# Kernel tuning notes

Measured on AMD Instinct MI355X. Metric: run time of the kernel, lower is better.

Reference implementation:

```python
import jax, jax.numpy as jnp
import numpy as np

N, C, K = 16384, 128, 20
C2, C8 = C // 2, C // 8
EPS = 1e-5  # torch BatchNorm default eps


def _bn(x, g, b, m, v):
    # inference-mode batchnorm over last (channel) axis
    return (x - m) * jax.lax.rsqrt(v + EPS) * g + b


def setup_inputs() -> dict:
    key = jax.random.key(0)
    ks = jax.random.split(key, 24)
    r = lambda i, sh, s=0.05: jax.random.normal(ks[i], sh, dtype=jnp.float32) * s
    u = lambda i, sh: jax.random.uniform(ks[i], sh, dtype=jnp.float32)
    return {
        "xyz": jax.random.normal(ks[0], (1, 3, N), dtype=jnp.float32),
        "features": jax.random.normal(ks[1], (1, C, N), dtype=jnp.float32),
        "w_mlp1": r(2, (C2, 6), 0.3), "b_mlp1": r(3, (C2,)),
        "bn1_g": u(4, (C2,)) * 0.5 + 0.75, "bn1_b": r(5, (C2,)),
        "bn1_m": r(6, (C2,)), "bn1_v": u(7, (C2,)) * 0.5 + 0.5,
        "w_mlp2": r(8, (C2, 2 * C), 0.06), "b_mlp2": r(9, (C2,)),
        "bn2_g": u(10, (C2,)) * 0.5 + 0.75, "bn2_b": r(11, (C2,)),
        "bn2_m": r(12, (C2,)), "bn2_v": u(13, (C2,)) * 0.5 + 0.5,
        "w_d1": r(14, (C8, C), 0.09), "w_d2": r(15, (C8, C), 0.09),
        "w_up": r(16, (C, C8), 0.25), "b_up": r(17, (C,)),
        "bnu_g": u(18, (C,)) * 0.5 + 0.75, "bnu_b": r(19, (C,)),
        "bnu_m": r(20, (C,)), "bnu_v": u(21, (C,)) * 0.5 + 0.5,
        "k": K,
    }


def reference(xyz, features, w_mlp1, b_mlp1, bn1_g, bn1_b, bn1_m, bn1_v,
              w_mlp2, b_mlp2, bn2_g, bn2_b, bn2_m, bn2_v,
              w_d1, w_d2, w_up, b_up, bnu_g, bnu_b, bnu_m, bnu_v, k):
    B = xyz.shape[0]
    xt = jnp.transpose(xyz, (0, 2, 1))        # [B,N,3]
    ft = jnp.transpose(features, (0, 2, 1))   # [B,N,C]
    # knn: pairwise_distance = -||xi||^2 + 2 xi.xj - ||xj||^2, topk = k nearest
    xx = jnp.sum(xyz * xyz, axis=1)           # [B,N]
    pd = 2.0 * jnp.einsum('bci,bcj->bij', xyz, xyz) - xx[:, :, None] - xx[:, None, :]
    _, idx = jax.lax.top_k(pd, k)             # [B,N,k]
    bidx = jnp.arange(B)[:, None, None]
    nbr_x = xt[bidx, idx]                     # [B,N,k,3]
    nbr_f = ft[bidx, idx]                     # [B,N,k,C]
    cx = xt[:, :, None, :]
    cf = ft[:, :, None, :]
    nx = jnp.concatenate([nbr_x - cx, jnp.broadcast_to(cx, nbr_x.shape)], axis=-1)  # [B,N,k,6]
    nf = jnp.concatenate([nbr_f - cf, jnp.broadcast_to(cf, nbr_f.shape)], axis=-1)  # [B,N,k,2C]
    hx = jax.nn.relu(_bn(jnp.einsum('bnkc,oc->bnko', nx, w_mlp1) + b_mlp1,
                         bn1_g, bn1_b, bn1_m, bn1_v))
    hf = jax.nn.relu(_bn(jnp.einsum('bnkc,oc->bnko', nf, w_mlp2) + b_mlp2,
                         bn2_g, bn2_b, bn2_m, bn2_v))
    f = jnp.max(jnp.concatenate([hx, hf], axis=-1), axis=2)   # [B,N,C]
    f1 = jax.nn.relu(jnp.einsum('bnc,oc->bno', f, w_d1))      # [B,N,C/8]
    f2 = jax.nn.relu(jnp.einsum('bnc,oc->bno', f, w_d2))      # [B,N,C/8]
    # faithful to original: .mean(...)[0] indexes batch 0 (valid since B==1)
    ch = jnp.mean(f1, axis=1)[0][:, None]     # [C/8,1]
    sp = jnp.mean(f2, axis=2)[0][None, :]     # [1,N]
    fe = jnp.sqrt(ch @ sp + 1e-12).T          # [N,C/8]
    fin = fe[None] + f1 + f2                  # [B,N,C/8]
    up = jax.nn.relu(_bn(jnp.einsum('bnc,oc->bno', fin, w_up) + b_up,
                         bnu_g, bnu_b, bnu_m, bnu_v))         # [B,N,C]
    fl = f - up
    fl = fl * jnp.tanh(jax.nn.softplus(fl))   # Mish
    return jnp.transpose(fl, (0, 2, 1))       # [B,C,N]
```

## Files before the change

### kernel.cpp

```cpp
#include <hip/hip_runtime.h>

#define NPT 16384
#define NEG_INF (-3.402823466e38f)

#define OFF_PTS4  0u
#define OFF_WKC   262144u
#define OFF_WAX   327680u
#define OFF_WBX   328704u
#define OFF_CBX   329728u
#define OFF_CBF   329984u
#define OFF_WUP   330240u
#define OFF_BUP   338432u
#define OFF_TAU   338944u
#define OFF_KNN   666624u
#define OFF_CH    1993728u
#define OFF_R     1994240u

__device__ __forceinline__ float pd_score(float qx2, float qy2, float qz2, float4 c) {
    return fmaf(qx2, c.x, fmaf(qy2, c.y, fmaf(qz2, c.z, -c.w)));
}

__device__ __forceinline__ unsigned sortable_f(float v) {
    unsigned b = __float_as_uint(v);
    return (b & 0x80000000u) ? ~b : (b | 0x80000000u);
}

__global__ __launch_bounds__(256) void kprep(
    const float* __restrict__ xyz,
    const float* __restrict__ w1, const float* __restrict__ b1,
    const float* __restrict__ g1, const float* __restrict__ bb1,
    const float* __restrict__ m1, const float* __restrict__ v1,
    const float* __restrict__ w2, const float* __restrict__ b2,
    const float* __restrict__ g2, const float* __restrict__ bb2,
    const float* __restrict__ m2, const float* __restrict__ v2,
    const float* __restrict__ wup, const float* __restrict__ bup,
    const float* __restrict__ gu, const float* __restrict__ bu2,
    const float* __restrict__ mu, const float* __restrict__ vu,
    float* __restrict__ wsf)
{
    const int tid = threadIdx.x;
    if (blockIdx.x == 0) {
        float* WKC = wsf + OFF_WKC/4;
        float* WAX = wsf + OFF_WAX/4;
        float* WBX = wsf + OFF_WBX/4;
        float* CBX = wsf + OFF_CBX/4;
        float* CBF = wsf + OFF_CBF/4;
        float* WUP = wsf + OFF_WUP/4;
        float* BUP = wsf + OFF_BUP/4;
        for (int i = tid; i < 16384; i += 256) {
            int c = i >> 7, o = i & 127, oo = o & 63;
            float s2 = g2[oo] * rsqrtf(v2[oo] + 1e-5f);
            float val = (o < 64) ? s2 * w2[oo*256 + c]
                                 : s2 * (w2[oo*256 + 128 + c] - w2[oo*256 + c]);
            WKC[c*128 + o] = val;
        }
        if (tid < 64) {
            int o = tid;
            float s1 = g1[o] * rsqrtf(v1[o] + 1e-5f);
            WAX[o*4+0] = s1 * w1[o*6+0];
            WAX[o*4+1] = s1 * w1[o*6+1];
            WAX[o*4+2] = s1 * w1[o*6+2];
            WAX[o*4+3] = 0.f;
            WBX[o*4+0] = s1 * (w1[o*6+3] - w1[o*6+0]);
            WBX[o*4+1] = s1 * (w1[o*6+4] - w1[o*6+1]);
            WBX[o*4+2] = s1 * (w1[o*6+5] - w1[o*6+2]);
            WBX[o*4+3] = 0.f;
            CBX[o] = s1 * b1[o] + (bb1[o] - m1[o]*s1);
            float s2b = g2[o] * rsqrtf(v2[o] + 1e-5f);
            CBF[o] = s2b * b2[o] + (bb2[o] - m2[o]*s2b);
        }
        if (tid < 128) {
            int o = tid;
            float su = gu[o] * rsqrtf(vu[o] + 1e-5f);
            for (int c = 0; c < 16; ++c) WUP[o*16+c] = su * wup[o*16+c];
            BUP[o] = su * bup[o] + (bu2[o] - mu[o]*su);
        }
    } else {
        #pragma clang fp contract(off)
        int n = (blockIdx.x - 1)*256 + tid;
        float x = xyz[n], y = xyz[NPT+n], z = xyz[2*NPT+n];
        float4 p; p.x = x; p.y = y; p.z = z;
        p.w = (x*x + y*y) + z*z;
        ((float4*)(wsf + OFF_PTS4/4))[n] = p;
    }
}

__global__ __launch_bounds__(256) void ktau(const float* __restrict__ wsf, float* __restrict__ tau)
{
    const float4* pts4 = (const float4*)(wsf + OFF_PTS4/4);
    __shared__ float t6[32][8][6];
    const int tid = threadIdx.x;
    const int ql = tid >> 3, t = tid & 7;
    const int q = blockIdx.x*32 + ql;
    float4 qp = pts4[q];
    float qx2 = qp.x + qp.x, qy2 = qp.y + qp.y, qz2 = qp.z + qp.z;
    float v0 = NEG_INF, v1 = NEG_INF, v2 = NEG_INF, v3 = NEG_INF, v4 = NEG_INF, v5 = NEG_INF;
    const int jb = t*128;
    for (int i = 0; i < 128; ++i) {
        float v = pd_score(qx2, qy2, qz2, pts4[jb + i]);
        float n5 = v > v5 ? (v > v4 ? v4 : v) : v5;
        float n4 = v > v4 ? (v > v3 ? v3 : v) : v4;
        float n3 = v > v3 ? (v > v2 ? v2 : v) : v3;
        float n2 = v > v2 ? (v > v1 ? v1 : v) : v2;
        float n1 = v > v1 ? (v > v0 ? v0 : v) : v1;
        float n0 = v > v0 ? v : v0;
        v0 = n0; v1 = n1; v2 = n2; v3 = n3; v4 = n4; v5 = n5;
    }
    t6[ql][t][0] = v0; t6[ql][t][1] = v1; t6[ql][t][2] = v2;
    t6[ql][t][3] = v3; t6[ql][t][4] = v4; t6[ql][t][5] = v5;
    __syncthreads();
    if (t == 0) {
        int p0=0,p1=0,p2=0,p3=0,p4=0,p5=0,p6=0,p7=0;
        float last = NEG_INF;
        for (int it = 0; it < 20; ++it) {
            float best = NEG_INF; int bl = -1;
#define CHK(L, PL) { float h = t6[ql][L][(PL) < 6 ? (PL) : 5]; if (((PL) < 6) && (h > best)) { best = h; bl = L; } }
            CHK(0,p0) CHK(1,p1) CHK(2,p2) CHK(3,p3) CHK(4,p4) CHK(5,p5) CHK(6,p6) CHK(7,p7)
#undef CHK
            p0 += (bl==0); p1 += (bl==1); p2 += (bl==2); p3 += (bl==3);
            p4 += (bl==4); p5 += (bl==5); p6 += (bl==6); p7 += (bl==7);
            last = best;
        }
        tau[q] = last - 5e-4f;
    }
}

__global__ __launch_bounds__(256) void kpush(const float* __restrict__ wsf,
                                             const float* __restrict__ tau,
                                             unsigned* __restrict__ bm)
{
    const float4* pts4 = (const float4*)(wsf + OFF_PTS4/4);
    __shared__ uint4 st[256][5];
    const int qg = blockIdx.x >> 5, c = blockIdx.x & 31;
    const int tid = threadIdx.x;
    const int jbase = c * 512;
    const int q = qg*256 + tid;
    float4 a = pts4[q];
    float ax2 = a.x + a.x, ay2 = a.y + a.y, az2 = a.z + a.z;
    float nt0 = -tau[q];
    for (int g = 0; g < 4; ++g) {
        unsigned wd[4];
#pragma unroll
        for (int u = 0; u < 4; ++u) {
            const int base = jbase + (g*4 + u)*32;
            unsigned w = 0u;
#pragma unroll
            for (int k = 0; k < 32; k += 4) {
                float4 d0 = pts4[base + k];
                float4 d1 = pts4[base + k + 1];
                float4 d2 = pts4[base + k + 2];
                float4 d3 = pts4[base + k + 3];
                float s0 = fmaf(az2, d0.z, fmaf(ay2, d0.y, fmaf(ax2, d0.x, nt0)));
                float s1 = fmaf(az2, d1.z, fmaf(ay2, d1.y, fmaf(ax2, d1.x, nt0)));
                float s2 = fmaf(az2, d2.z, fmaf(ay2, d2.y, fmaf(ax2, d2.x, nt0)));
                float s3 = fmaf(az2, d3.z, fmaf(ay2, d3.y, fmaf(ax2, d3.x, nt0)));
                w |= (s0 >= d0.w) ? (1u << k)       : 0u;
                w |= (s1 >= d1.w) ? (1u << (k + 1)) : 0u;
                w |= (s2 >= d2.w) ? (1u << (k + 2)) : 0u;
                w |= (s3 >= d3.w) ? (1u << (k + 3)) : 0u;
            }
            wd[u] = w;
        }
        uint4 o; o.x = wd[0]; o.y = wd[1]; o.z = wd[2]; o.w = wd[3];
        st[tid][g] = o;
    }
    uint4* dst = (uint4*)(bm + (size_t)q*512 + c*16);
#pragma unroll
    for (int g = 0; g < 4; ++g) dst[g] = st[tid][g];
}

#define KS(A,B) V##A = (kk > V##B) ? V##B : ((kk > V##A) ? kk : V##A);
__global__ __launch_bounds__(256) void ksel(const float* __restrict__ wsf,
                                            const unsigned* __restrict__ bm,
                                            unsigned* __restrict__ knn)
{
    #pragma clang fp contract(off)
    const float4* pts4 = (const float4*)(wsf + OFF_PTS4/4);
    __shared__ unsigned short spool[4][1024];
    __shared__ unsigned long long pool[4][128];
    const int lane = threadIdx.x & 63;
    const int qw   = threadIdx.x >> 6;
    const int q = blockIdx.x*4 + qw;
    float4 qp = pts4[q];

    const uint4* row = (const uint4*)(bm + (size_t)q*512) + lane*2;
    uint4 a0 = row[0], a1 = row[1];
    unsigned wv[8] = {a0.x, a0.y, a0.z, a0.w, a1.x, a1.y, a1.z, a1.w};
    int scnt = 0;
#pragma unroll
    for (int t = 0; t < 8; ++t) scnt += __popc(wv[t]);
    int spre = scnt;
#pragma unroll
    for (int o = 1; o < 64; o <<= 1) {
        int t2 = __shfl_up(spre, o, 64);
        spre += (lane >= o) ? t2 : 0;
    }
    int nS = __shfl(spre, 63, 64);
    if (nS > 1024) nS = 1024;
    unsigned short* sp = spool[qw];
    int wptr = spre - scnt;
#pragma unroll
    for (int t = 0; t < 8; ++t) {
        unsigned w = wv[t];
        const int wbase = (lane*8 + t)*32;
        while (w) {
            int b = __ffs(w) - 1; w &= w - 1;
            if (wptr < 1024) sp[wptr] = (unsigned short)(wbase + b);
            ++wptr;
        }
    }
    __syncthreads();

    unsigned long long V0=0,V1=0,V2=0,V3=0,V4=0,V5=0,V6=0,V7=0;
    const int rounds = (nS + 63) >> 6;
    for (int r = 0; r < rounds; ++r) {
        int i = r*64 + lane;
        bool val = i < nS;
        int j = val ? (int)sp[i] : 0;
        float4 cp = pts4[j];
        float d  = (qp.x*cp.x + qp.y*cp.y) + qp.z*cp.z;
        float pd = (2.0f*d - qp.w) - cp.w;
        unsigned long long kk = val ? (((unsigned long long)sortable_f(pd) << 14)
                                      | (unsigned long long)(16383 - j)) : 0ull;
        if (kk > V7) {
            KS(7,6) KS(6,5) KS(5,4) KS(4,3) KS(3,2) KS(2,1) KS(1,0)
            V0 = (kk > V0) ? kk : V0;
        }
    }

    unsigned long long ss = V0;
#pragma unroll
    for (int k = 2; k <= 64; k <<= 1) {
#pragma unroll
        for (int j = k >> 1; j > 0; j >>= 1) {
            unsigned long long o = __shfl_xor(ss, j, 64);
            bool up = ((lane & k) == 0);
            bool lower = ((lane & j) == 0);
            ss = (lower == up) ? ((ss < o) ? ss : o) : ((ss > o) ? ss : o);
        }
    }
    unsigned long long theta = __shfl(ss, 44, 64);

    int kcnt = (int)(V0 >= theta) + (int)(V1 >= theta) + (int)(V2 >= theta)
             + (int)(V3 >= theta) + (int)(V4 >= theta) + (int)(V5 >= theta)
             + (int)(V6 >= theta) + (int)(V7 >= theta);
    int ksc = kcnt;
#pragma unroll
    for (int o = 1; o < 64; o <<= 1) {
        int t2 = __shfl_up(ksc, o, 64);
        ksc += (lane >= o) ? t2 : 0;
    }
    int C = __shfl(ksc, 63, 64);
    int kbase = ksc - kcnt;
    if (C > 128) C = 128;
    unsigned long long* pq = pool[qw];
#define WPOOL(I, VI) if (I < kcnt) { int p = kbase + I; if (p < 128) pq[p] = VI; }
    WPOOL(0, V0) WPOOL(1, V1) WPOOL(2, V2) WPOOL(3, V3)
    WPOOL(4, V4) WPOOL(5, V5) WPOOL(6, V6) WPOOL(7, V7)
#undef WPOOL
    __syncthreads();

    bool h1 = lane < C;
    bool h2 = (lane + 64) < C;
    unsigned long long k1 = h1 ? pq[lane] : 0ull;
    unsigned long long k2 = h2 ? pq[lane + 64] : 0ull;
    int r1 = 0, r2 = 0;
    for (int i = 0; i < C; ++i) {
        unsigned long long ki = pq[i];
        r1 += (int)(ki > k1);
        r2 += (int)(ki > k2);
    }
    unsigned* kout = knn + (size_t)q*20;
    if (h1 && r1 < 20) kout[r1] = 16383u - (unsigned)(k1 & 0x3FFFull);
    if (h2 && r2 < 20) kout[r2] = 16383u - (unsigned)(k2 & 0x3FFFull);
}

__global__ __launch_bounds__(256) void kgemm(const float* __restrict__ feat,
                                             const float* __restrict__ wsf,
                                             float* __restrict__ G, float* __restrict__ T2)
{
    __shared__ float As[32][32];
    __shared__ float Bs[32][128];
    const float* WKC = wsf + OFF_WKC/4;
    const float* CBF = wsf + OFF_CBF/4;
    const int tid = threadIdx.x;
    const int n0 = blockIdx.x * 32;
    const int tx = tid & 15, ty = tid >> 4;
    float acc[2][8] = {};
    for (int kc = 0; kc < 4; ++kc) {
        int c0 = kc * 32;
        for (int i = tid; i < 1024; i += 256) {
            int cl = i >> 5, nl = i & 31;
            As[cl][nl] = feat[(size_t)(c0 + cl)*NPT + n0 + nl];
        }
        for (int i = tid; i < 4096; i += 256) {
            int cl = i >> 7, ol = i & 127;
            Bs[cl][ol] = WKC[(c0 + cl)*128 + ol];
        }
        __syncthreads();
        for (int cc = 0; cc < 32; ++cc) {
            float av[2], bv[8];
#pragma unroll
            for (int r = 0; r < 2; ++r) av[r] = As[cc][ty*2 + r];
#pragma unroll
            for (int s = 0; s < 8; ++s) bv[s] = Bs[cc][tx*8 + s];
#pragma unroll
            for (int r = 0; r < 2; ++r)
#pragma unroll
                for (int s = 0; s < 8; ++s)
                    acc[r][s] = fmaf(av[r], bv[s], acc[r][s]);
        }
        __syncthreads();
    }
#pragma unroll
    for (int r = 0; r < 2; ++r) {
        int n = n0 + ty*2 + r;
        if (tx < 8) {
            float* dst = G + (size_t)n*128 + 64 + tx*8;
#pragma unroll
            for (int s = 0; s < 8; ++s) dst[s] = acc[r][s];
        } else {
            int ob = (tx - 8)*8;
            float* dst = T2 + (size_t)n*128 + 64 + ob;
#pragma unroll
            for (int s = 0; s < 8; ++s) dst[s] = acc[r][s] + CBF[ob + s];
        }
    }
}

__global__ __launch_bounds__(256) void kxpart(const float* __restrict__ xyz,
                                              const float* __restrict__ wsf,
                                              float* __restrict__ G, float* __restrict__ T2)
{
    const float4* WAX = (const float4*)(wsf + OFF_WAX/4);
    const float4* WBX = (const float4*)(wsf + OFF_WBX/4);
    const float*  CBX = wsf + OFF_CBX/4;
    const int tid = threadIdx.x;
    const int o = tid & 63;
    const int n = blockIdx.x*4 + (tid >> 6);
    float x = xyz[n], y = xyz[NPT+n], z = xyz[2*NPT+n];
    float4 A = WAX[o], B = WBX[o];
    G[(size_t)n*128 + o]  = fmaf(x, A.x, fmaf(y, A.y, z*A.z));
    T2[(size_t)n*128 + o] = fmaf(x, B.x, fmaf(y, B.y, fmaf(z, B.z, CBX[o])));
}

__global__ __launch_bounds__(256) void kgather(const float* __restrict__ wsf,
                                               const unsigned* __restrict__ knn,
                                               const float* __restrict__ G,
                                               const float* __restrict__ T2,
                                               const float* __restrict__ wd1,
                                               const float* __restrict__ wd2,
                                               float* __restrict__ F, float* __restrict__ F1,
                                               float* __restrict__ F2, float* __restrict__ SPm,
                                               float* __restrict__ PART)
{
    __shared__ float fsh[32][136];
    __shared__ float w1s[16][136];
    __shared__ float w2s[16][136];
    __shared__ float f1sh[32][16];
    __shared__ float f2p[32][8];
    const int tid = threadIdx.x;
    for (int i = tid; i < 2048; i += 256) {
        int o = i >> 7, cc = i & 127;
        w1s[o][cc] = wd1[i];
        w2s[o][cc] = wd2[i];
    }
    const int nl = tid >> 3, qt = tid & 7;
    const int n = blockIdx.x*32 + nl;
    const unsigned* ip = knn + (size_t)n*20;
    float acc[16];
#pragma unroll
    for (int e = 0; e < 16; ++e) acc[e] = NEG_INF;
    for (int k = 0; k < 20; ++k) {
        unsigned j = ip[k];
        const float4* g4 = (const float4*)(G + (size_t)j*128 + qt*16);
#pragma unroll
        for (int r = 0; r < 4; ++r) {
            float4 gv = g4[r];
            acc[r*4+0] = fmaxf(acc[r*4+0], gv.x);
            acc[r*4+1] = fmaxf(acc[r*4+1], gv.y);
            acc[r*4+2] = fmaxf(acc[r*4+2], gv.z);
            acc[r*4+3] = fmaxf(acc[r*4+3], gv.w);
        }
    }
    const float4* t4 = (const float4*)(T2 + (size_t)n*128 + qt*16);
    float4* fg = (float4*)(F + (size_t)n*128 + qt*16);
    float4* fs = (float4*)&fsh[nl][qt*16];
#pragma unroll
    for (int r = 0; r < 4; ++r) {
        float4 tv = t4[r];
        float4 o4;
        o4.x = fmaxf(acc[r*4+0] + tv.x, 0.f);
        o4.y = fmaxf(acc[r*4+1] + tv.y, 0.f);
        o4.z = fmaxf(acc[r*4+2] + tv.z, 0.f);
        o4.w = fmaxf(acc[r*4+3] + tv.w, 0.f);
        fg[r] = o4; fs[r] = o4;
    }
    __syncthreads();
    float a1[2] = {0,0}, a2[2] = {0,0};
    const int ob = qt*2;
    for (int c4 = 0; c4 < 32; ++c4) {
        float4 fv = ((const float4*)&fsh[nl][0])[c4];
#pragma unroll
        for (int r = 0; r < 2; ++r) {
            float4 wv1 = ((const float4*)&w1s[ob + r][0])[c4];
            float4 wv2 = ((const float4*)&w2s[ob + r][0])[c4];
            a1[r] = fmaf(fv.x, wv1.x, fmaf(fv.y, wv1.y, fmaf(fv.z, wv1.z, fmaf(fv.w, wv1.w, a1[r]))));
            a2[r] = fmaf(fv.x, wv2.x, fmaf(fv.y, wv2.y, fmaf(fv.z, wv2.z, fmaf(fv.w, wv2.w, a2[r]))));
        }
    }
    float s2sum = 0.f;
#pragma unroll
    for (int r = 0; r < 2; ++r) {
        a1[r] = fmaxf(a1[r], 0.f);
        a2[r] = fmaxf(a2[r], 0.f);
        s2sum += a2[r];
        F1[(size_t)n*16 + ob + r] = a1[r];
        F2[(size_t)n*16 + ob + r] = a2[r];
        f1sh[nl][ob + r] = a1[r];
    }
    f2p[nl][qt] = s2sum;
    __syncthreads();
    if (qt == 0) {
        float s = 0.f;
#pragma unroll
        for (int t = 0; t < 8; ++t) s += f2p[nl][t];
        SPm[n] = s * (1.0f/16.0f);
    }
    if (tid < 16) {
        float s = 0.f;
        for (int r = 0; r < 32; ++r) s += f1sh[r][tid];
        PART[blockIdx.x*16 + tid] = s;
    }
}

__global__ __launch_bounds__(64) void kch(const float* __restrict__ PART, float* __restrict__ CH)
{
    const int tid = threadIdx.x;
    if (tid < 16) {
        float s = 0.f;
        for (int b = 0; b < 512; ++b) s += PART[b*16 + tid];
        CH[tid] = s * (1.0f/16384.0f);
    }
}

__global__ __launch_bounds__(256) void kfinal(const float* __restrict__ wsf,
                                              const float* __restrict__ F,
                                              const float* __restrict__ F1,
                                              const float* __restrict__ F2,
                                              const float* __restrict__ SPm,
                                              const float* __restrict__ CH,
                                              float* __restrict__ out)
{
    const float* WUP = wsf + OFF_WUP/4;
    const float* BUP = wsf + OFF_BUP/4;
    const int tid = threadIdx.x;
    const int nl = tid >> 2, qt = tid & 3;
    const int n = blockIdx.x*64 + nl;
    float spv = SPm[n];
    float fin[16];
    const float4* f14 = (const float4*)(F1 + (size_t)n*16);
    const float4* f24 = (const float4*)(F2 + (size_t)n*16);
#pragma unroll
    for (int c4 = 0; c4 < 4; ++c4) {
        float4 a = f14[c4], b = f24[c4];
        fin[c4*4+0] = sqrtf(fmaf(CH[c4*4+0], spv, 1e-12f)) + a.x + b.x;
        fin[c4*4+1] = sqrtf(fmaf(CH[c4*4+1], spv, 1e-12f)) + a.y + b.y;
        fin[c4*4+2] = sqrtf(fmaf(CH[c4*4+2], spv, 1e-12f)) + a.z + b.z;
        fin[c4*4+3] = sqrtf(fmaf(CH[c4*4+3], spv, 1e-12f)) + a.w + b.w;
    }
    const float4* fF = (const float4*)(F + (size_t)n*128);
    for (int o4 = qt*8; o4 < qt*8 + 8; ++o4) {
        float4 fv = fF[o4];
        float fa[4] = {fv.x, fv.y, fv.z, fv.w};
#pragma unroll
        for (int e = 0; e < 4; ++e) {
            int o = o4*4 + e;
            float u = BUP[o];
#pragma unroll
            for (int c = 0; c < 16; ++c) u = fmaf(fin[c], WUP[o*16 + c], u);
            u = fmaxf(u, 0.f);
            float fl = fa[e] - u;
            float flc = fminf(fl, 15.f);
            float t = expf(flc);
            float w = 1.f + t;
            float w2 = w*w;
            float th = (w2 - 1.f) / (w2 + 1.f);
            float res = (fl > 15.f) ? fl : fl * th;
            out[(size_t)o*NPT + n] = res;
        }
    }
}

extern "C" void kernel_launch(void* const* d_in, const int* in_sizes, int n_in,
                              void* d_out, int out_size, void* d_ws, size_t ws_size,
                              hipStream_t stream) {
    const float* xyz  = (const float*)d_in[0];
    const float* feat = (const float*)d_in[1];
    const float* w1   = (const float*)d_in[2];
    const float* b1   = (const float*)d_in[3];
    const float* g1   = (const float*)d_in[4];
    const float* bb1  = (const float*)d_in[5];
    const float* m1   = (const float*)d_in[6];
    const float* v1   = (const float*)d_in[7];
    const float* w2   = (const float*)d_in[8];
    const float* b2   = (const float*)d_in[9];
    const float* g2   = (const float*)d_in[10];
    const float* bb2  = (const float*)d_in[11];
    const float* m2   = (const float*)d_in[12];
    const float* v2   = (const float*)d_in[13];
    const float* wd1  = (const float*)d_in[14];
    const float* wd2  = (const float*)d_in[15];
    const float* wup  = (const float*)d_in[16];
    const float* bup  = (const float*)d_in[17];
    const float* gu   = (const float*)d_in[18];
    const float* bu2  = (const float*)d_in[19];
    const float* mu   = (const float*)d_in[20];
    const float* vu   = (const float*)d_in[21];
    float* out = (float*)d_out;

    float* wsf = (float*)d_ws;
    unsigned* bm   = (unsigned*)((char*)d_ws + OFF_R);
    unsigned* knn  = (unsigned*)((char*)d_ws + OFF_KNN);
    float* TAU  = (float*)((char*)d_ws + OFF_TAU);
    float* PART = (float*)((char*)d_ws + OFF_TAU);
    float* CH   = (float*)((char*)d_ws + OFF_CH);
    float* G  = (float*)((char*)d_ws + OFF_R);
    float* T2 = G  + 2097152;
    float* F  = T2 + 2097152;
    float* F1 = F  + 2097152;
    float* F2 = F1 + 262144;
    float* SPm = F2 + 262144;

    kprep<<<dim3(65),  dim3(256), 0, stream>>>(xyz, w1,b1,g1,bb1,m1,v1,
                                               w2,b2,g2,bb2,m2,v2,
                                               wup,bup,gu,bu2,mu,vu, wsf);
    ktau <<<dim3(512), dim3(256), 0, stream>>>(wsf, TAU);
    kpush<<<dim3(2048), dim3(256), 0, stream>>>(wsf, TAU, bm);
    ksel <<<dim3(4096), dim3(256), 0, stream>>>(wsf, bm, knn);
    kgemm<<<dim3(512), dim3(256), 0, stream>>>(feat, wsf, G, T2);
    kxpart<<<dim3(4096), dim3(256), 0, stream>>>(xyz, wsf, G, T2);
    kgather<<<dim3(512), dim3(256), 0, stream>>>(wsf, knn, G, T2, wd1, wd2, F, F1, F2, SPm, PART);
    kch  <<<dim3(1),   dim3(64), 0, stream>>>(PART, CH);
    kfinal<<<dim3(256), dim3(256), 0, stream>>>(wsf, F, F1, F2, SPm, CH, out);
}
```

Before: 219.8 us.

## Store gathered neighbor projections in bf16 and fuse xyz part into GEMM

The per-point projection table G that kgather reads for every one of the 20 neighbors is now stored as bf16 instead of fp32. This halves the bytes of the dominant random-gather traffic. The separate kxpart kernel is folded into the tail of kgemm, which removes one launch and one pass over G and T2. The cost is bf16 rounding on the max-pooled features, which may affect accuracy tolerance.

```diff
diff --git a/kernel.cpp b/kernel.cpp
--- a/kernel.cpp
+++ b/kernel.cpp
@@ -24,6 +24,13 @@
     unsigned b = __float_as_uint(v);
     return (b & 0x80000000u) ? ~b : (b | 0x80000000u);
 }
+
+__device__ __forceinline__ unsigned short f2bf(float f) {
+    unsigned b = __float_as_uint(f);
+    return (unsigned short)((b + 0x7FFFu + ((b >> 16) & 1u)) >> 16);
+}
+#define BF2F_LO(w) __uint_as_float((w) << 16)
+#define BF2F_HI(w) __uint_as_float((w) & 0xFFFF0000u)
 
 __global__ __launch_bounds__(256) void kprep(
     const float* __restrict__ xyz,
@@ -277,7 +284,8 @@
 
 __global__ __launch_bounds__(256) void kgemm(const float* __restrict__ feat,
                                              const float* __restrict__ wsf,
-                                             float* __restrict__ G, float* __restrict__ T2)
+                                             unsigned short* __restrict__ Gb,
+                                             float* __restrict__ T2)
 {
     __shared__ float As[32][32];
     __shared__ float Bs[32][128];
@@ -316,9 +324,12 @@
     for (int r = 0; r < 2; ++r) {
         int n = n0 + ty*2 + r;
         if (tx < 8) {
-            float* dst = G + (size_t)n*128 + 64 + tx*8;
-#pragma unroll
-            for (int s = 0; s < 8; ++s) dst[s] = acc[r][s];
+            unsigned pk[4];
+#pragma unroll
+            for (int s = 0; s < 4; ++s)
+                pk[s] = (unsigned)f2bf(acc[r][2*s]) | ((unsigned)f2bf(acc[r][2*s+1]) << 16);
+            uint4 o4; o4.x = pk[0]; o4.y = pk[1]; o4.z = pk[2]; o4.w = pk[3];
+            *(uint4*)(Gb + (size_t)n*128 + 64 + tx*8) = o4;
         } else {
             int ob = (tx - 8)*8;
             float* dst = T2 + (size_t)n*128 + 64 + ob;
@@ -326,27 +337,27 @@
             for (int s = 0; s < 8; ++s) dst[s] = acc[r][s] + CBF[ob + s];
         }
     }
-}
-
-__global__ __launch_bounds__(256) void kxpart(const float* __restrict__ xyz,
-                                              const float* __restrict__ wsf,
-                                              float* __restrict__ G, float* __restrict__ T2)
-{
-    const float4* WAX = (const float4*)(wsf + OFF_WAX/4);
-    const float4* WBX = (const float4*)(wsf + OFF_WBX/4);
-    const float*  CBX = wsf + OFF_CBX/4;
-    const int tid = threadIdx.x;
+    const float4* pts4 = (const float4*)(wsf + OFF_PTS4/4);
+    const float4* WAX4 = (const float4*)(wsf + OFF_WAX/4);
+    const float4* WBX4 = (const float4*)(wsf + OFF_WBX/4);
+    const float*  CBX  = wsf + OFF_CBX/4;
     const int o = tid & 63;
-    const int n = blockIdx.x*4 + (tid >> 6);
-    float x = xyz[n], y = xyz[NPT+n], z = xyz[2*NPT+n];
-    float4 A = WAX[o], B = WBX[o];
-    G[(size_t)n*128 + o]  = fmaf(x, A.x, fmaf(y, A.y, z*A.z));
-    T2[(size_t)n*128 + o] = fmaf(x, B.x, fmaf(y, B.y, fmaf(z, B.z, CBX[o])));
+    float4 A = WAX4[o], B = WBX4[o];
+    float cb = CBX[o];
+#pragma unroll
+    for (int r = 0; r < 8; ++r) {
+        int n = n0 + r*4 + (tid >> 6);
+        float4 p = pts4[n];
+        float gv = fmaf(p.x, A.x, fmaf(p.y, A.y, p.z*A.z));
+        float tv = fmaf(p.x, B.x, fmaf(p.y, B.y, fmaf(p.z, B.z, cb)));
+        Gb[(size_t)n*128 + o] = f2bf(gv);
+        T2[(size_t)n*128 + o] = tv;
+    }
 }
 
 __global__ __launch_bounds__(256) void kgather(const float* __restrict__ wsf,
                                                const unsigned* __restrict__ knn,
-                                               const float* __restrict__ G,
+                                               const unsigned short* __restrict__ Gb,
                                                const float* __restrict__ T2,
                                                const float* __restrict__ wd1,
                                                const float* __restrict__ wd2,
@@ -373,15 +384,16 @@
     for (int e = 0; e < 16; ++e) acc[e] = NEG_INF;
     for (int k = 0; k < 20; ++k) {
         unsigned j = ip[k];
-        const float4* g4 = (const float4*)(G + (size_t)j*128 + qt*16);
-#pragma unroll
-        for (int r = 0; r < 4; ++r) {
-            float4 gv = g4[r];
-            acc[r*4+0] = fmaxf(acc[r*4+0], gv.x);
-            acc[r*4+1] = fmaxf(acc[r*4+1], gv.y);
-            acc[r*4+2] = fmaxf(acc[r*4+2], gv.z);
-            acc[r*4+3] = fmaxf(acc[r*4+3], gv.w);
-        }
+        const uint4* g4 = (const uint4*)(Gb + (size_t)j*128 + qt*16);
+        uint4 w0 = g4[0], w1 = g4[1];
+        acc[0]  = fmaxf(acc[0],  BF2F_LO(w0.x)); acc[1]  = fmaxf(acc[1],  BF2F_HI(w0.x));
+        acc[2]  = fmaxf(acc[2],  BF2F_LO(w0.y)); acc[3]  = fmaxf(acc[3],  BF2F_HI(w0.y));
+        acc[4]  = fmaxf(acc[4],  BF2F_LO(w0.z)); acc[5]  = fmaxf(acc[5],  BF2F_HI(w0.z));
+        acc[6]  = fmaxf(acc[6],  BF2F_LO(w0.w)); acc[7]  = fmaxf(acc[7],  BF2F_HI(w0.w));
+        acc[8]  = fmaxf(acc[8],  BF2F_LO(w1.x)); acc[9]  = fmaxf(acc[9],  BF2F_HI(w1.x));
+        acc[10] = fmaxf(acc[10], BF2F_LO(w1.y)); acc[11] = fmaxf(acc[11], BF2F_HI(w1.y));
+        acc[12] = fmaxf(acc[12], BF2F_LO(w1.z)); acc[13] = fmaxf(acc[13], BF2F_HI(w1.z));
+        acc[14] = fmaxf(acc[14], BF2F_LO(w1.w)); acc[15] = fmaxf(acc[15], BF2F_HI(w1.w));
     }
     const float4* t4 = (const float4*)(T2 + (size_t)n*128 + qt*16);
     float4* fg = (float4*)(F + (size_t)n*128 + qt*16);
@@ -525,8 +537,8 @@
     float* TAU  = (float*)((char*)d_ws + OFF_TAU);
     float* PART = (float*)((char*)d_ws + OFF_TAU);
     float* CH   = (float*)((char*)d_ws + OFF_CH);
-    float* G  = (float*)((char*)d_ws + OFF_R);
-    float* T2 = G  + 2097152;
+    unsigned short* Gb = (unsigned short*)((char*)d_ws + OFF_R);
+    float* T2 = (float*)((char*)d_ws + OFF_R + 4194304);
     float* F  = T2 + 2097152;
     float* F1 = F  + 2097152;
     float* F2 = F1 + 262144;
@@ -538,9 +550,8 @@
     ktau <<<dim3(512), dim3(256), 0, stream>>>(wsf, TAU);
     kpush<<<dim3(2048), dim3(256), 0, stream>>>(wsf, TAU, bm);
     ksel <<<dim3(4096), dim3(256), 0, stream>>>(wsf, bm, knn);
-    kgemm<<<dim3(512), dim3(256), 0, stream>>>(feat, wsf, G, T2);
-    kxpart<<<dim3(4096), dim3(256), 0, stream>>>(xyz, wsf, G, T2);
-    kgather<<<dim3(512), dim3(256), 0, stream>>>(wsf, knn, G, T2, wd1, wd2, F, F1, F2, SPm, PART);
+    kgemm<<<dim3(512), dim3(256), 0, stream>>>(feat, wsf, Gb, T2);
+    kgather<<<dim3(512), dim3(256), 0, stream>>>(wsf, knn, Gb, T2, wd1, wd2, F, F1, F2, SPm, PART);
     kch  <<<dim3(1),   dim3(64), 0, stream>>>(PART, CH);
     kfinal<<<dim3(256), dim3(256), 0, stream>>>(wsf, F, F1, F2, SPm, CH, out);
 }
```

New measurement: 215.2 us. 2.1% less time.
